# Optimization experiments

Hardware: AMD Instinct MI355X
Metric: run time of the kernel (lower is better)

## Reference

```python
import jax, jax.numpy as jnp
import numpy as np

B, T, C = 2, 8192, 1024
H, BS, LW = 16, 64, 128          # num_heads, block_size, local_window_size
D = C // H                        # head_dim = 64
W = BS + LW                       # max window length per block = 192
NB = T // BS                      # number of blocks


def setup_inputs() -> dict:
    key = jax.random.key(0)
    ks = jax.random.split(key, 11)
    s = 1.0 / np.sqrt(C)          # small init so softmax is not saturated
    return {
        'query': jax.random.normal(ks[0], (B, T, C), jnp.float32),
        'key':   jax.random.normal(ks[1], (B, T, C), jnp.float32),
        'value': jax.random.normal(ks[2], (B, T, C), jnp.float32),
        'Wq': jax.random.normal(ks[3], (C, C), jnp.float32) * s,
        'bq': jax.random.normal(ks[4], (C,), jnp.float32) * s,
        'Wk': jax.random.normal(ks[5], (C, C), jnp.float32) * s,
        'bk': jax.random.normal(ks[6], (C,), jnp.float32) * s,
        'Wv': jax.random.normal(ks[7], (C, C), jnp.float32) * s,
        'bv': jax.random.normal(ks[8], (C,), jnp.float32) * s,
        'Wo': jax.random.normal(ks[9], (C, C), jnp.float32) * s,
        'bo': jax.random.normal(ks[10], (C,), jnp.float32) * s,
    }


def reference(query, key, value, Wq, bq, Wk, bk, Wv, bv, Wo, bo):
    # projections -> (B, H, T, D)
    def proj(x, Wt, bt):
        return (x @ Wt.T + bt).reshape(B, T, H, D).transpose(0, 2, 1, 3)

    scale = jnp.asarray(D, query.dtype) ** -0.5
    q = proj(query, Wq, bq) * scale
    k = proj(key, Wk, bk)
    v = proj(value, Wv, bv)

    # per-block window indices: block i attends to [i - LW//2, i + BS + LW//2)
    starts = jnp.arange(NB) * BS                              # (NB,)
    idx = starts[:, None] + jnp.arange(-LW // 2, BS + LW // 2)  # (NB, W)
    valid = (idx >= 0) & (idx < T)                            # (NB, W)
    cidx = jnp.clip(idx, 0, T - 1)

    q_blk = q.reshape(B, H, NB, BS, D)
    k_win = k[:, :, cidx, :]                                  # (B, H, NB, W, D)
    v_win = v[:, :, cidx, :]

    scores = jnp.einsum('bhnqd,bhnkd->bhnqk', q_blk, k_win).astype(jnp.float32)
    scores = jnp.where(valid[None, None, :, None, :], scores, -jnp.inf)
    probs = jax.nn.softmax(scores, axis=-1).astype(q.dtype)

    out = jnp.einsum('bhnqk,bhnkd->bhnqd', probs, v_win)      # (B, H, NB, BS, D)
    out = out.reshape(B, H, T, D).transpose(0, 2, 1, 3).reshape(B, T, C)
    return out @ Wo.T + bo
```

## Files before the change

kernel.cpp:

```cpp
#include <hip/hip_runtime.h>
#include <hip/hip_bf16.h>
#include <type_traits>

#define BATCH 2
#define SEQ   8192
#define CH    1024
#define NH    16
#define BLK   64
#define WIN   192
#define NBL   128
#define DH    64
#define MR    (BATCH*SEQ)

typedef __bf16 bf16x8 __attribute__((ext_vector_type(8)));
typedef float  f32x4  __attribute__((ext_vector_type(4)));

__device__ __forceinline__ f32x4 zero4() {
    f32x4 z; z[0]=0.f; z[1]=0.f; z[2]=0.f; z[3]=0.f; return z;
}

union Pack4 { __hip_bfloat16 h[4]; uint2 u; };
union Pack8 { __hip_bfloat16 h[8]; uint4 u; };

typedef const __attribute__((address_space(1))) unsigned int* gas_ptr;
typedef       __attribute__((address_space(3))) unsigned int* las_ptr;

__device__ __forceinline__ void gload_lds16(const __hip_bfloat16* g, __hip_bfloat16* l) {
    __builtin_amdgcn_global_load_lds((gas_ptr)(const void*)g, (las_ptr)(void*)l, 16, 0, 0);
}

__global__ __launch_bounds__(256) void pack_bf16(
    const float* __restrict__ src, __hip_bfloat16* __restrict__ dst, int n8)
{
    int i = blockIdx.x * 256 + threadIdx.x;
    if (i >= n8) return;
    const float4* s = reinterpret_cast<const float4*>(src);
    float4 a = s[2 * i], b = s[2 * i + 1];
    Pack8 p;
    p.h[0] = __float2bfloat16(a.x); p.h[1] = __float2bfloat16(a.y);
    p.h[2] = __float2bfloat16(a.z); p.h[3] = __float2bfloat16(a.w);
    p.h[4] = __float2bfloat16(b.x); p.h[5] = __float2bfloat16(b.y);
    p.h[6] = __float2bfloat16(b.z); p.h[7] = __float2bfloat16(b.w);
    reinterpret_cast<uint4*>(dst)[i] = p.u;
}

template<typename OT>
__global__ __launch_bounds__(256) void gemm_bt_bf16(
    const __hip_bfloat16* __restrict__ A, const __hip_bfloat16* __restrict__ Wb,
    const float* __restrict__ bias, OT* __restrict__ out, float alpha)
{
    __shared__ alignas(16) __hip_bfloat16 As[128 * 32];
    __shared__ alignas(16) __hip_bfloat16 Bs[128 * 32];

    const int tid  = threadIdx.x;
    const int m0   = blockIdx.y * 128;
    const int n0   = blockIdx.x * 128;
    const int wid  = tid >> 6;
    const int lane = tid & 63;
    const int quad = lane >> 4;
    const int l16  = lane & 15;
    const int wr   = wid >> 1, wc = wid & 1;

    const int r0 = tid >> 2;
    const int sg = (tid & 3) * 8;
    const __hip_bfloat16* a0 = A  + (size_t)(m0 + r0)      * CH + sg;
    const __hip_bfloat16* a1 = A  + (size_t)(m0 + r0 + 64) * CH + sg;
    const __hip_bfloat16* b0 = Wb + (size_t)(n0 + r0)      * CH + sg;
    const __hip_bfloat16* b1 = Wb + (size_t)(n0 + r0 + 64) * CH + sg;
    __hip_bfloat16* la0 = As + tid * 8;
    __hip_bfloat16* la1 = As + (tid + 256) * 8;
    __hip_bfloat16* lb0 = Bs + tid * 8;
    __hip_bfloat16* lb1 = Bs + (tid + 256) * 8;

    f32x4 acc[4][4];
    #pragma unroll
    for (int i = 0; i < 4; i++)
        #pragma unroll
        for (int j = 0; j < 4; j++) acc[i][j] = zero4();

    for (int k0 = 0; k0 < CH; k0 += 32) {
        gload_lds16(a0 + k0, la0);
        gload_lds16(a1 + k0, la1);
        gload_lds16(b0 + k0, lb0);
        gload_lds16(b1 + k0, lb1);
        __syncthreads();

        bf16x8 af[4], bfr[4];
        #pragma unroll
        for (int i = 0; i < 4; i++)
            af[i] = *reinterpret_cast<const bf16x8*>(
                As + (wr * 64 + i * 16 + l16) * 32 + quad * 8);
        #pragma unroll
        for (int j = 0; j < 4; j++)
            bfr[j] = *reinterpret_cast<const bf16x8*>(
                Bs + (wc * 64 + j * 16 + l16) * 32 + quad * 8);
        #pragma unroll
        for (int i = 0; i < 4; i++)
            #pragma unroll
            for (int j = 0; j < 4; j++)
                acc[i][j] = __builtin_amdgcn_mfma_f32_16x16x32_bf16(
                    af[i], bfr[j], acc[i][j], 0, 0, 0);
        __syncthreads();
    }

    #pragma unroll
    for (int j = 0; j < 4; j++) {
        const int col = n0 + wc * 64 + j * 16 + l16;
        const float bv = bias[col];
        #pragma unroll
        for (int i = 0; i < 4; i++) {
            #pragma unroll
            for (int r = 0; r < 4; r++) {
                const int row = m0 + wr * 64 + i * 16 + quad * 4 + r;
                float v = alpha * (acc[i][j][r] + bv);
                if constexpr (std::is_same<OT, float>::value)
                    out[(size_t)row * CH + col] = v;
                else
                    out[(size_t)row * CH + col] = __float2bfloat16(v);
            }
        }
    }
}

__global__ __launch_bounds__(256) void attn_kernel(
    const __hip_bfloat16* __restrict__ qg,
    const __hip_bfloat16* __restrict__ kg,
    const __hip_bfloat16* __restrict__ vg,
    __hip_bfloat16* __restrict__ ctx)
{
    __shared__ alignas(16) char smem[62464];
    auto qs = reinterpret_cast<__hip_bfloat16(*)[72]>(smem);
    auto ks = reinterpret_cast<__hip_bfloat16(*)[72]>(smem + 9216);
    auto vt = reinterpret_cast<__hip_bfloat16(*)[200]>(smem + 36864);
    auto ps = reinterpret_cast<__hip_bfloat16(*)[200]>(smem);

    const int blk = blockIdx.x;
    const int n = blk & (NBL - 1);
    const int h = (blk >> 7) & (NH - 1);
    const int b = blk >> 11;
    const int t0  = n * BLK;
    const int kst = t0 - 64;
    const int tid = threadIdx.x;
    const size_t baseBH = (size_t)b * SEQ * CH + (size_t)h * DH;

    #pragma unroll
    for (int it = 0; it < 2; it++) {
        int c = tid + it * 256;
        int row = c >> 3, seg = c & 7;
        *reinterpret_cast<uint4*>(&qs[row][seg * 8]) =
            *reinterpret_cast<const uint4*>(qg + baseBH + (size_t)(t0 + row) * CH + seg * 8);
    }
    #pragma unroll
    for (int it = 0; it < 6; it++) {
        int c = tid + it * 256;
        int row = c >> 3, seg = c & 7;
        int tr = kst + row; tr = tr < 0 ? 0 : (tr >= SEQ ? SEQ - 1 : tr);
        *reinterpret_cast<uint4*>(&ks[row][seg * 8]) =
            *reinterpret_cast<const uint4*>(kg + baseBH + (size_t)tr * CH + seg * 8);
    }
    #pragma unroll
    for (int it = 0; it < 6; it++) {
        int c = tid + it * 256;
        int j = c % WIN, seg = c / WIN;
        int tr = kst + j; tr = tr < 0 ? 0 : (tr >= SEQ ? SEQ - 1 : tr);
        Pack8 p;
        p.u = *reinterpret_cast<const uint4*>(vg + baseBH + (size_t)tr * CH + seg * 8);
        #pragma unroll
        for (int e = 0; e < 8; e++) vt[seg * 8 + e][j] = p.h[e];
    }
    __syncthreads();

    const int wid = tid >> 6, lane = tid & 63, quad = lane >> 4, l16 = lane & 15;

    f32x4 sc[12];
    #pragma unroll
    for (int j = 0; j < 12; j++) sc[j] = zero4();
    #pragma unroll
    for (int kk = 0; kk < 2; kk++) {
        bf16x8 aq = *reinterpret_cast<const bf16x8*>(&qs[wid * 16 + l16][kk * 32 + quad * 8]);
        #pragma unroll
        for (int j = 0; j < 12; j++) {
            bf16x8 bk = *reinterpret_cast<const bf16x8*>(&ks[j * 16 + l16][kk * 32 + quad * 8]);
            sc[j] = __builtin_amdgcn_mfma_f32_16x16x32_bf16(aq, bk, sc[j], 0, 0, 0);
        }
    }
    __syncthreads();

    #pragma unroll
    for (int r = 0; r < 4; r++) {
        float s[12];
        float mx = -3.0e38f;
        #pragma unroll
        for (int j = 0; j < 12; j++) {
            int col = j * 16 + l16;
            int tr = kst + col;
            bool valid = (tr >= 0) && (tr < SEQ);
            s[j] = valid ? sc[j][r] : -3.0e38f;
            mx = fmaxf(mx, s[j]);
        }
        #pragma unroll
        for (int o = 1; o < 16; o <<= 1) mx = fmaxf(mx, __shfl_xor(mx, o, 64));
        float sum = 0.f;
        #pragma unroll
        for (int j = 0; j < 12; j++) {
            float e = __expf(s[j] - mx);
            s[j] = e;
            sum += e;
        }
        #pragma unroll
        for (int o = 1; o < 16; o <<= 1) sum += __shfl_xor(sum, o, 64);
        const float inv = 1.f / sum;
        const int row = wid * 16 + quad * 4 + r;
        #pragma unroll
        for (int j = 0; j < 12; j++)
            ps[row][j * 16 + l16] = __float2bfloat16(s[j] * inv);
    }
    __syncthreads();

    f32x4 oa[4];
    #pragma unroll
    for (int j = 0; j < 4; j++) oa[j] = zero4();
    #pragma unroll
    for (int kk = 0; kk < 6; kk++) {
        bf16x8 ap = *reinterpret_cast<const bf16x8*>(&ps[wid * 16 + l16][kk * 32 + quad * 8]);
        #pragma unroll
        for (int j = 0; j < 4; j++) {
            bf16x8 bv = *reinterpret_cast<const bf16x8*>(&vt[j * 16 + l16][kk * 32 + quad * 8]);
            oa[j] = __builtin_amdgcn_mfma_f32_16x16x32_bf16(ap, bv, oa[j], 0, 0, 0);
        }
    }
    #pragma unroll
    for (int j = 0; j < 4; j++) {
        const int d = j * 16 + l16;
        #pragma unroll
        for (int r = 0; r < 4; r++) {
            const int i = wid * 16 + quad * 4 + r;
            ctx[baseBH + (size_t)(t0 + i) * CH + d] = __float2bfloat16(oa[j][r]);
        }
    }
}

extern "C" void kernel_launch(void* const* d_in, const int* in_sizes, int n_in,
                              void* d_out, int out_size, void* d_ws, size_t ws_size,
                              hipStream_t stream)
{
    const float* query = (const float*)d_in[0];
    const float* key_i = (const float*)d_in[1];
    const float* value = (const float*)d_in[2];
    const float* Wq = (const float*)d_in[3];
    const float* bq = (const float*)d_in[4];
    const float* Wk = (const float*)d_in[5];
    const float* bk = (const float*)d_in[6];
    const float* Wv = (const float*)d_in[7];
    const float* bv = (const float*)d_in[8];
    const float* Wo = (const float*)d_in[9];
    const float* bo = (const float*)d_in[10];
    float* out = (float*)d_out;

    const size_t NELEM = (size_t)MR * CH;
    const size_t WELEM = (size_t)CH * CH;

    __hip_bfloat16* S0 = (__hip_bfloat16*)d_ws;
    __hip_bfloat16* S1 = S0 + NELEM;
    __hip_bfloat16* S2 = S1 + NELEM;
    __hip_bfloat16* S3 = S2 + NELEM;
    __hip_bfloat16* wqb = S3;
    __hip_bfloat16* wkb = S3 + WELEM;
    __hip_bfloat16* wvb = S3 + 2 * WELEM;
    __hip_bfloat16* wob = S3 + 3 * WELEM;

    __hip_bfloat16* xq = (__hip_bfloat16*)d_out;
    __hip_bfloat16* xk = xq + NELEM;
    __hip_bfloat16* vb = (__hip_bfloat16*)d_out;
    __hip_bfloat16* qb = S1;
    __hip_bfloat16* kb = S2;
    __hip_bfloat16* cb = S0;

    const int nA8 = (int)(NELEM / 8);
    const int nW8 = (int)(WELEM / 8);

    pack_bf16<<<nA8 / 256, 256, 0, stream>>>(query, xq, nA8);
    pack_bf16<<<nA8 / 256, 256, 0, stream>>>(key_i, xk, nA8);
    pack_bf16<<<nA8 / 256, 256, 0, stream>>>(value, S0, nA8);
    pack_bf16<<<nW8 / 256, 256, 0, stream>>>(Wq, wqb, nW8);
    pack_bf16<<<nW8 / 256, 256, 0, stream>>>(Wk, wkb, nW8);
    pack_bf16<<<nW8 / 256, 256, 0, stream>>>(Wv, wvb, nW8);
    pack_bf16<<<nW8 / 256, 256, 0, stream>>>(Wo, wob, nW8);

    dim3 ggrid(CH / 128, MR / 128);
    const float qscale = 0.125f;

    gemm_bt_bf16<__hip_bfloat16><<<ggrid, 256, 0, stream>>>(xq, wqb, bq, qb, qscale);
    gemm_bt_bf16<__hip_bfloat16><<<ggrid, 256, 0, stream>>>(xk, wkb, bk, kb, 1.0f);
    gemm_bt_bf16<__hip_bfloat16><<<ggrid, 256, 0, stream>>>(S0, wvb, bv, vb, 1.0f);

    attn_kernel<<<BATCH * NH * NBL, 256, 0, stream>>>(qb, kb, vb, cb);

    gemm_bt_bf16<float><<<ggrid, 256, 0, stream>>>(cb, wob, bo, out, 1.0f);
}
```

Baseline: 529.7 us.

## Double GEMM K-tile to 64, XOR-swizzle LDS, and merge Q/K projections

After: 501.8 us. 5.3% less time.

```diff
diff --git a/kernel.cpp b/kernel.cpp
--- a/kernel.cpp
+++ b/kernel.cpp
@@ -19,7 +19,6 @@
     f32x4 z; z[0]=0.f; z[1]=0.f; z[2]=0.f; z[3]=0.f; return z;
 }
 
-union Pack4 { __hip_bfloat16 h[4]; uint2 u; };
 union Pack8 { __hip_bfloat16 h[8]; uint4 u; };
 
 typedef const __attribute__((address_space(1))) unsigned int* gas_ptr;
@@ -45,13 +44,11 @@
 }
 
 template<typename OT>
-__global__ __launch_bounds__(256) void gemm_bt_bf16(
+__device__ __forceinline__ void gemm_body(
     const __hip_bfloat16* __restrict__ A, const __hip_bfloat16* __restrict__ Wb,
-    const float* __restrict__ bias, OT* __restrict__ out, float alpha)
-{
-    __shared__ alignas(16) __hip_bfloat16 As[128 * 32];
-    __shared__ alignas(16) __hip_bfloat16 Bs[128 * 32];
-
+    const float* __restrict__ bias, OT* __restrict__ out, float alpha,
+    __hip_bfloat16* As, __hip_bfloat16* Bs)
+{
     const int tid  = threadIdx.x;
     const int m0   = blockIdx.y * 128;
     const int n0   = blockIdx.x * 128;
@@ -61,16 +58,15 @@
     const int l16  = lane & 15;
     const int wr   = wid >> 1, wc = wid & 1;
 
-    const int r0 = tid >> 2;
-    const int sg = (tid & 3) * 8;
-    const __hip_bfloat16* a0 = A  + (size_t)(m0 + r0)      * CH + sg;
-    const __hip_bfloat16* a1 = A  + (size_t)(m0 + r0 + 64) * CH + sg;
-    const __hip_bfloat16* b0 = Wb + (size_t)(n0 + r0)      * CH + sg;
-    const __hip_bfloat16* b1 = Wb + (size_t)(n0 + r0 + 64) * CH + sg;
-    __hip_bfloat16* la0 = As + tid * 8;
-    __hip_bfloat16* la1 = As + (tid + 256) * 8;
-    __hip_bfloat16* lb0 = Bs + tid * 8;
-    __hip_bfloat16* lb1 = Bs + (tid + 256) * 8;
+    int offA[4], offB[4];
+    #pragma unroll
+    for (int it = 0; it < 4; it++) {
+        int c = tid + it * 256;
+        int r = c >> 3;
+        int s = (c & 7) ^ (r & 7);
+        offA[it] = (m0 + r) * CH + s * 8;
+        offB[it] = (n0 + r) * CH + s * 8;
+    }
 
     f32x4 acc[4][4];
     #pragma unroll
@@ -78,28 +74,37 @@
         #pragma unroll
         for (int j = 0; j < 4; j++) acc[i][j] = zero4();
 
-    for (int k0 = 0; k0 < CH; k0 += 32) {
-        gload_lds16(a0 + k0, la0);
-        gload_lds16(a1 + k0, la1);
-        gload_lds16(b0 + k0, lb0);
-        gload_lds16(b1 + k0, lb1);
+    for (int k0 = 0; k0 < CH; k0 += 64) {
+        #pragma unroll
+        for (int it = 0; it < 4; it++)
+            gload_lds16(A + offA[it] + k0, As + (tid + it * 256) * 8);
+        #pragma unroll
+        for (int it = 0; it < 4; it++)
+            gload_lds16(Wb + offB[it] + k0, Bs + (tid + it * 256) * 8);
         __syncthreads();
 
-        bf16x8 af[4], bfr[4];
-        #pragma unroll
-        for (int i = 0; i < 4; i++)
-            af[i] = *reinterpret_cast<const bf16x8*>(
-                As + (wr * 64 + i * 16 + l16) * 32 + quad * 8);
-        #pragma unroll
-        for (int j = 0; j < 4; j++)
-            bfr[j] = *reinterpret_cast<const bf16x8*>(
-                Bs + (wc * 64 + j * 16 + l16) * 32 + quad * 8);
-        #pragma unroll
-        for (int i = 0; i < 4; i++)
+        #pragma unroll
+        for (int kk = 0; kk < 2; kk++) {
+            bf16x8 af[4], bfr[4];
             #pragma unroll
-            for (int j = 0; j < 4; j++)
-                acc[i][j] = __builtin_amdgcn_mfma_f32_16x16x32_bf16(
-                    af[i], bfr[j], acc[i][j], 0, 0, 0);
+            for (int i = 0; i < 4; i++) {
+                int r = wr * 64 + i * 16 + l16;
+                int chunk = r * 8 + ((kk * 4 + quad) ^ (l16 & 7));
+                af[i] = *reinterpret_cast<const bf16x8*>(As + chunk * 8);
+            }
+            #pragma unroll
+            for (int j = 0; j < 4; j++) {
+                int r = wc * 64 + j * 16 + l16;
+                int chunk = r * 8 + ((kk * 4 + quad) ^ (l16 & 7));
+                bfr[j] = *reinterpret_cast<const bf16x8*>(Bs + chunk * 8);
+            }
+            #pragma unroll
+            for (int i = 0; i < 4; i++)
+                #pragma unroll
+                for (int j = 0; j < 4; j++)
+                    acc[i][j] = __builtin_amdgcn_mfma_f32_16x16x32_bf16(
+                        af[i], bfr[j], acc[i][j], 0, 0, 0);
+        }
         __syncthreads();
     }
 
@@ -120,6 +125,30 @@
             }
         }
     }
+}
+
+__global__ __launch_bounds__(256) void gemm_qk(
+    const __hip_bfloat16* __restrict__ A0, const __hip_bfloat16* __restrict__ W0,
+    const float* __restrict__ b0, __hip_bfloat16* __restrict__ o0, float alpha0,
+    const __hip_bfloat16* __restrict__ A1, const __hip_bfloat16* __restrict__ W1,
+    const float* __restrict__ b1, __hip_bfloat16* __restrict__ o1)
+{
+    __shared__ alignas(16) __hip_bfloat16 As[128 * 64];
+    __shared__ alignas(16) __hip_bfloat16 Bs[128 * 64];
+    if (blockIdx.z == 0)
+        gemm_body<__hip_bfloat16>(A0, W0, b0, o0, alpha0, As, Bs);
+    else
+        gemm_body<__hip_bfloat16>(A1, W1, b1, o1, 1.0f, As, Bs);
+}
+
+template<typename OT>
+__global__ __launch_bounds__(256) void gemm_one(
+    const __hip_bfloat16* __restrict__ A, const __hip_bfloat16* __restrict__ Wb,
+    const float* __restrict__ bias, OT* __restrict__ out)
+{
+    __shared__ alignas(16) __hip_bfloat16 As[128 * 64];
+    __shared__ alignas(16) __hip_bfloat16 Bs[128 * 64];
+    gemm_body<OT>(A, Wb, bias, out, 1.0f, As, Bs);
 }
 
 __global__ __launch_bounds__(256) void attn_kernel(
@@ -288,13 +317,13 @@
     pack_bf16<<<nW8 / 256, 256, 0, stream>>>(Wo, wob, nW8);
 
     dim3 ggrid(CH / 128, MR / 128);
-    const float qscale = 0.125f;
-
-    gemm_bt_bf16<__hip_bfloat16><<<ggrid, 256, 0, stream>>>(xq, wqb, bq, qb, qscale);
-    gemm_bt_bf16<__hip_bfloat16><<<ggrid, 256, 0, stream>>>(xk, wkb, bk, kb, 1.0f);
-    gemm_bt_bf16<__hip_bfloat16><<<ggrid, 256, 0, stream>>>(S0, wvb, bv, vb, 1.0f);
+    dim3 qkgrid(CH / 128, MR / 128, 2);
+
+    gemm_qk<<<qkgrid, 256, 0, stream>>>(xq, wqb, bq, qb, 0.125f,
+                                        xk, wkb, bk, kb);
+    gemm_one<__hip_bfloat16><<<ggrid, 256, 0, stream>>>(S0, wvb, bv, vb);
 
     attn_kernel<<<BATCH * NH * NBL, 256, 0, stream>>>(qb, kb, vb, cb);
 
-    gemm_bt_bf16<float><<<ggrid, 256, 0, stream>>>(cb, wob, bo, out, 1.0f);
-}
+    gemm_one<float><<<ggrid, 256, 0, stream>>>(cb, wob, bo, out);
+}
```
